# Performance work log

Hardware: AMD Instinct MI355X
Metric: run time of the kernel (lower is better)

The kernel has to match this reference:

```python
import jax, jax.numpy as jnp
import numpy as np

N_NODES = 100000
N_EDGES = 1600000
IN_C, HID, OUT_C = 16, 64, 1


def setup_inputs() -> dict:
    key = jax.random.key(0)
    ks = jax.random.split(key, 12)
    x = jax.random.normal(ks[0], (N_NODES, IN_C), dtype=jnp.float32)
    edge_index = jax.random.randint(ks[1], (2, N_EDGES), 0, N_NODES, dtype=jnp.int32)

    def lin(k, fan_in, fan_out):
        s = 1.0 / np.sqrt(fan_in)
        kw, kb = jax.random.split(k)
        W = jax.random.uniform(kw, (fan_in, fan_out), jnp.float32, -s, s)
        b = jax.random.uniform(kb, (fan_out,), jnp.float32, -s, s)
        return W, b

    W0, b0 = lin(ks[2], IN_C, HID)      # node_mlps[0]
    W1, b1 = lin(ks[3], HID, HID)       # node_mlps[1]
    W2, b2 = lin(ks[4], HID, OUT_C)     # node_mlps[2]
    M0, bM0 = lin(ks[5], 2 * HID, HID)  # message_mlps[0] (only one used for num_layers=3)
    return {"x": x, "edge_index": edge_index, "W0": W0, "b0": b0,
            "W1": W1, "b1": b1, "W2": W2, "b2": b2, "M0": M0, "bM0": bM0}


def _message_passing(h, src, dst, M, bM):
    # gather -> concat -> linear -> scatter-add -> degree normalize
    msgs = jnp.concatenate([h[src], h[dst]], axis=1) @ M + bM  # [E, HID]
    agg = jax.ops.segment_sum(msgs, dst, num_segments=N_NODES)  # [N, HID]
    deg = jax.ops.segment_sum(jnp.ones((src.shape[0],), h.dtype), dst,
                              num_segments=N_NODES)
    deg = jnp.clip(deg, 1.0, None)[:, None]
    return agg / deg


def reference(x, edge_index, W0, b0, W1, b1, W2, b2, M0, bM0):
    src, dst = edge_index[0], edge_index[1]
    h = jax.nn.relu(x @ W0 + b0)                  # node_mlps[0] (dropout = eval identity)
    h = h + _message_passing(h, src, dst, M0, bM0)
    h = jax.nn.relu(h @ W1 + b1)                  # node_mlps[1]
    return h @ W2 + b2                            # node_mlps[2], [N, 1]
```

## Files before the change

### kernel.cpp

```cpp
#include <hip/hip_runtime.h>

#define HID 64
#define IN_C 16

typedef __attribute__((ext_vector_type(8))) short short8;
typedef __attribute__((ext_vector_type(4))) float f32x4;

__device__ __forceinline__ float bitsf(unsigned u) { return __uint_as_float(u); }
__device__ __forceinline__ unsigned rne16(float f) {
    unsigned u = __float_as_uint(f);
    return (u + 0x7fffu + ((u >> 16) & 1u)) >> 16;
}
__device__ __forceinline__ float lanebcf(float v, int l) {
    return __int_as_float(__builtin_amdgcn_readlane(__float_as_int(v), l));
}
__device__ __forceinline__ float f4c(const float4& a, int c) {
    switch (c & 3) { case 0: return a.x; case 1: return a.y; case 2: return a.z; default: return a.w; }
}

__global__ void k_init(const float* __restrict__ M0, const float* __restrict__ W1,
                       const float* __restrict__ bM0, const float* __restrict__ b1,
                       ushort* __restrict__ WPhi, ushort* __restrict__ WPlo,
                       float* __restrict__ bias192) {
    int tid = blockIdx.x * 256 + threadIdx.x;
    if (tid >= 64 * 192) return;
    int cc = tid % 192;
    int k  = tid / 192;
    float w;
    if (cc < 64) {
        float a = 0.f;
#pragma unroll
        for (int m = 0; m < HID; ++m) a = fmaf(M0[k * HID + m], W1[m * HID + cc], a);
        w = a;
    } else if (cc < 128) {
        int c = cc - 64;
        float a = W1[k * HID + c];
#pragma unroll
        for (int m = 0; m < HID; ++m) a = fmaf(M0[(HID + k) * HID + m], W1[m * HID + c], a);
        w = a;
    } else {
        w = W1[k * HID + (cc - 128)];
    }
    unsigned wb = __float_as_uint(w);
    ushort hi = (ushort)(wb >> 16);
    float hif = __uint_as_float(wb & 0xffff0000u);
    ushort lo = (ushort)(__float_as_uint(w - hif) >> 16);
    int ct = cc >> 4, s = k >> 5, l = ((k >> 3) & 3) * 16 + (cc & 15), j = k & 7;
    int fi = ((ct * 2 + s) * 64 + l) * 8 + j;
    WPhi[fi] = hi;
    WPlo[fi] = lo;
    if (k == 0) {
        float bv;
        if (cc < 64) bv = 0.f;
        else if (cc < 128) {
            int c = cc - 64;
            float a = b1[c];
#pragma unroll
            for (int m = 0; m < HID; ++m) a = fmaf(bM0[m], W1[m * HID + c], a);
            bv = a;
        } else bv = b1[cc - 128];
        bias192[cc] = bv;
    }
}

__global__ __launch_bounds__(256) void k_pre_hist(
    const float* __restrict__ x, const float* __restrict__ W0, const float* __restrict__ b0,
    const ushort* __restrict__ WPhi, const ushort* __restrict__ WPlo,
    const float* __restrict__ bias192,
    ushort* __restrict__ zb, float* __restrict__ PQ, float* __restrict__ Pp, int N,
    const int* __restrict__ ei, int* __restrict__ bhT, int E, int B1, int NB1)
{
    __shared__ ushort hhi[64 * 64];
    __shared__ ushort hlo[64 * 64];

    if ((int)blockIdx.x < NB1) {
        int* h = reinterpret_cast<int*>(hhi);
        for (int i = threadIdx.x; i < B1; i += 256) h[i] = 0;
        __syncthreads();
        int CH = (E + NB1 - 1) / NB1;
        int e0 = blockIdx.x * CH;
        int e1 = min(e0 + CH, E);
        for (int e = e0 + (int)threadIdx.x; e < e1; e += 256)
            atomicAdd(&h[ei[E + e] >> 8], 1);
        __syncthreads();
        for (int i = threadIdx.x; i < B1; i += 256)
            bhT[(size_t)i * NB1 + blockIdx.x] = h[i];
        return;
    }

    int tid  = threadIdx.x;
    int lane = tid & 63;
    int w    = tid >> 6;
    int n0   = (blockIdx.x - NB1) * 64;

    float w0c[IN_C];
#pragma unroll
    for (int k = 0; k < IN_C; ++k) w0c[k] = W0[k * HID + lane];
    float b0l = b0[lane];

    short8 Whi[3][2], Wlo[3][2];
    float4 bias4[3];
#pragma unroll
    for (int i = 0; i < 3; ++i) {
        int ct = w * 3 + i;
#pragma unroll
        for (int s = 0; s < 2; ++s) {
            int fi = ((ct * 2 + s) * 64 + lane) * 8;
            Whi[i][s] = *reinterpret_cast<const short8*>(WPhi + fi);
            Wlo[i][s] = *reinterpret_cast<const short8*>(WPlo + fi);
        }
        bias4[i] = *reinterpret_cast<const float4*>(bias192 + ct * 16 + (lane >> 4) * 4);
    }

    int nx = n0 + w * 16 + (lane >> 2);
    float4 xq = make_float4(0.f, 0.f, 0.f, 0.f);
    if (nx < N) xq = *reinterpret_cast<const float4*>(x + (size_t)nx * IN_C + (lane & 3) * 4);

#pragma unroll
    for (int nn = 0; nn < 16; ++nn) {
        float acc = b0l;
#pragma unroll
        for (int k = 0; k < IN_C; ++k)
            acc = fmaf(lanebcf(f4c(xq, k & 3), 4 * nn + (k >> 2)), w0c[k], acc);
        float h = fmaxf(acc, 0.f);
        unsigned hb = __float_as_uint(h);
        ushort hi = (ushort)(hb >> 16);
        float hif = __uint_as_float(hb & 0xffff0000u);
        ushort lo = (ushort)(__float_as_uint(h - hif) >> 16);
        int nl = w * 16 + nn;
        int u  = ((lane >> 3) ^ (nl & 7));
        int off = nl * 64 + u * 8 + (lane & 7);
        hhi[off] = hi;
        hlo[off] = lo;
    }
    __syncthreads();

#pragma unroll
    for (int st = 0; st < 4; ++st) {
        int nloc = st * 16 + (lane & 15);
        short8 Ahi[2], Alo[2];
#pragma unroll
        for (int s = 0; s < 2; ++s) {
            int u = (s * 4 + (lane >> 4)) ^ (nloc & 7);
            int off = nloc * 64 + u * 8;
            Ahi[s] = *reinterpret_cast<const short8*>(hhi + off);
            Alo[s] = *reinterpret_cast<const short8*>(hlo + off);
        }
        int n = n0 + st * 16 + (lane & 15);
#pragma unroll
        for (int i = 0; i < 3; ++i) {
            int ct = w * 3 + i;
            f32x4 acc = {bias4[i].x, bias4[i].y, bias4[i].z, bias4[i].w};
#pragma unroll
            for (int s = 0; s < 2; ++s) {
                acc = __builtin_amdgcn_mfma_f32_16x16x32_bf16(Whi[i][s], Ahi[s], acc, 0, 0, 0);
                acc = __builtin_amdgcn_mfma_f32_16x16x32_bf16(Whi[i][s], Alo[s], acc, 0, 0, 0);
                acc = __builtin_amdgcn_mfma_f32_16x16x32_bf16(Wlo[i][s], Ahi[s], acc, 0, 0, 0);
                acc = __builtin_amdgcn_mfma_f32_16x16x32_bf16(Wlo[i][s], Alo[s], acc, 0, 0, 0);
            }
            if (n < N) {
                int chb = ct * 16 + (lane >> 4) * 4;
                if (chb < 64) {
                    uint2 pk;
                    pk.x = rne16(acc[0]) | (rne16(acc[1]) << 16);
                    pk.y = rne16(acc[2]) | (rne16(acc[3]) << 16);
                    *reinterpret_cast<uint2*>(zb + (size_t)n * HID + chb) = pk;
                } else if (chb < 128) {
                    float4 v = make_float4(acc[0], acc[1], acc[2], acc[3]);
                    *reinterpret_cast<float4*>(PQ + (size_t)n * HID + (chb - 64)) = v;
                } else {
                    float4 v = make_float4(acc[0], acc[1], acc[2], acc[3]);
                    *reinterpret_cast<float4*>(Pp + (size_t)n * HID + (chb - 128)) = v;
                }
            }
        }
    }
}

__global__ void k_scan1(const int* __restrict__ cnt, int* __restrict__ rs,
                        int* __restrict__ bsum, int M) {
    __shared__ int lds[256];
    int t = threadIdx.x;
    int base = blockIdx.x * 4096 + t * 16;
    int v[16];
    if (base + 16 <= M) {
#pragma unroll
        for (int u = 0; u < 4; ++u) {
            int4 w = *reinterpret_cast<const int4*>(cnt + base + u * 4);
            v[u * 4 + 0] = w.x; v[u * 4 + 1] = w.y; v[u * 4 + 2] = w.z; v[u * 4 + 3] = w.w;
        }
    } else {
#pragma unroll
        for (int u = 0; u < 16; ++u) v[u] = (base + u < M) ? cnt[base + u] : 0;
    }
    int run = 0;
#pragma unroll
    for (int u = 0; u < 16; ++u) { int tv = v[u]; v[u] = run; run += tv; }
    lds[t] = run;
    __syncthreads();
#pragma unroll
    for (int off = 1; off < 256; off <<= 1) {
        int xw = (t >= off) ? lds[t - off] : 0;
        __syncthreads();
        lds[t] += xw;
        __syncthreads();
    }
    int excl = lds[t] - run;
    if (t == 255) bsum[blockIdx.x] = lds[255];
#pragma unroll
    for (int u = 0; u < 16; ++u)
        if (base + u < M) rs[base + u] = excl + v[u];
}

__global__ void k_scan_add(int* __restrict__ rs, const int* __restrict__ bsum,
                           int NB, int M, int E) {
    __shared__ int lds[256];
    __shared__ int excl[256];
    int t = threadIdx.x;
    int v = (t < NB) ? bsum[t] : 0;
    lds[t] = v;
    __syncthreads();
#pragma unroll
    for (int off = 1; off < 256; off <<= 1) {
        int xw = (t >= off) ? lds[t - off] : 0;
        __syncthreads();
        lds[t] += xw;
        __syncthreads();
    }
    excl[t] = lds[t] - v;
    __syncthreads();
    int i = blockIdx.x * 256 + t;
    if (i < M) rs[i] += excl[i >> 12];
    if (i == 0) rs[M] = E;
}

__global__ __launch_bounds__(256) void k_p1scat(const int* __restrict__ ei, const int* __restrict__ off,
                                                unsigned* __restrict__ tmp, int E, int B1) {
    __shared__ int cur[1024];
    int NB1 = gridDim.x;
    for (int i = threadIdx.x; i < B1; i += 256)
        cur[i] = off[(size_t)i * NB1 + blockIdx.x];
    __syncthreads();
    int CH = (E + NB1 - 1) / NB1;
    int e0 = blockIdx.x * CH;
    int e1 = min(e0 + CH, E);
    for (int e = e0 + (int)threadIdx.x; e < e1; e += 256) {
        int s = ei[e];
        int d = ei[E + e];
        int pos = atomicAdd(&cur[d >> 8], 1);
        tmp[pos] = (unsigned)s | ((unsigned)(d & 255) << 24);
    }
}

__global__ __launch_bounds__(256) void k_p2(const unsigned* __restrict__ tmp, const int* __restrict__ off,
                                            int* __restrict__ rs, int* __restrict__ csr,
                                            int E, int N, int B1, int NB1) {
    __shared__ int h2[256];
    __shared__ int sc[256];
    __shared__ int cur[256];
    int b = blockIdx.x;
    int t = threadIdx.x;
    int bb0 = off[(size_t)b * NB1];
    int bb1 = off[(size_t)(b + 1) * NB1];

    h2[t] = 0;
    __syncthreads();
    for (int i = bb0 + t; i < bb1; i += 256)
        atomicAdd(&h2[tmp[i] >> 24], 1);
    __syncthreads();

    int v = h2[t];
    sc[t] = v;
    __syncthreads();
#pragma unroll
    for (int o = 1; o < 256; o <<= 1) {
        int xw = (t >= o) ? sc[t - o] : 0;
        __syncthreads();
        sc[t] += xw;
        __syncthreads();
    }
    int excl = sc[t] - v;

    int node = b * 256 + t;
    if (node < N) rs[node] = bb0 + excl;
    if (b == B1 - 1 && t == 0) rs[N] = E;
    cur[t] = bb0 + excl;
    __syncthreads();

    for (int i = bb0 + t; i < bb1; i += 256) {
        unsigned ed = tmp[i];
        int pos = atomicAdd(&cur[ed >> 24], 1);
        csr[pos] = (int)(ed & 0x00FFFFFFu);
    }
}

__global__ __launch_bounds__(256) void k_final(
    const ushort* __restrict__ zb, const float* __restrict__ PQ, const float* __restrict__ Pp,
    const int* __restrict__ rs, const int* __restrict__ csr,
    const float* __restrict__ W2, const float* __restrict__ b2,
    float* __restrict__ out, int N)
{
    int lane = threadIdx.x & 63;
    int g    = lane >> 4;
    int ql   = lane & 15;
    int oct  = ql & 7;
    int half = ql >> 3;
    int wid  = (blockIdx.x * 256 + threadIdx.x) >> 6;
    int nw   = (gridDim.x * 256) >> 6;

    int c0 = oct * 8 + half * 4;
    float4 w2v = *reinterpret_cast<const float4*>(W2 + c0);
    float b2s = b2[0];

    for (int n0 = wid * 4; n0 < N; n0 += nw * 4) {
        int ng   = n0 + g;
        bool okg = ng < N;

        int rv = okg ? rs[ng + half] : 0;
        int beg = __shfl(rv, g * 16 + 0);
        int end = __shfl(rv, g * 16 + 8);
        int deg = end - beg;
        int md = deg;
        md = max(md, __shfl_xor(md, 16));
        md = max(md, __shfl_xor(md, 32));

        float acc[8];
#pragma unroll
        for (int i = 0; i < 8; ++i) acc[i] = 0.f;

        for (int c = 0; c < md; c += 32) {
            int j0 = c + ql, j1 = c + 16 + ql;
            int ia = (j0 < deg) ? csr[beg + j0] : -1;
            int ib = (j1 < deg) ? csr[beg + j1] : -1;
#pragma unroll
            for (int tb = 0; tb < 4; ++tb) {
                if (tb > 0 && md <= c + 8 * tb) break;
                int srcs[4];
#pragma unroll
                for (int t4 = 0; t4 < 4; ++t4) {
                    int t = tb * 4 + t4;
                    int e = 2 * t + half;
                    srcs[t4] = __shfl(tb < 2 ? ia : ib, g * 16 + (e & 15));
                }
                uint4 rw[4];
#pragma unroll
                for (int t4 = 0; t4 < 4; ++t4) {
                    int s = srcs[t4] < 0 ? 0 : srcs[t4];
                    rw[t4] = *reinterpret_cast<const uint4*>(zb + (size_t)s * HID + oct * 8);
                }
#pragma unroll
                for (int t4 = 0; t4 < 4; ++t4) {
                    if (srcs[t4] >= 0) {
                        uint4 wv = rw[t4];
                        acc[0] += bitsf(wv.x << 16); acc[1] += bitsf(wv.x & 0xffff0000u);
                        acc[2] += bitsf(wv.y << 16); acc[3] += bitsf(wv.y & 0xffff0000u);
                        acc[4] += bitsf(wv.z << 16); acc[5] += bitsf(wv.z & 0xffff0000u);
                        acc[6] += bitsf(wv.w << 16); acc[7] += bitsf(wv.w & 0xffff0000u);
                    }
                }
            }
        }
#pragma unroll
        for (int i = 0; i < 8; ++i) acc[i] += __shfl_xor(acc[i], 8);

        float s0 = half ? acc[4] : acc[0];
        float s1 = half ? acc[5] : acc[1];
        float s2 = half ? acc[6] : acc[2];
        float s3 = half ? acc[7] : acc[3];

        float4 base = make_float4(0.f, 0.f, 0.f, 0.f);
        if (okg) {
            base = *reinterpret_cast<const float4*>(PQ + (size_t)ng * HID + c0);
            if (deg == 0)
                base = *reinterpret_cast<const float4*>(Pp + (size_t)ng * HID + c0);
        }
        float rcpd = (deg > 0) ? (1.f / (float)deg) : 0.f;
        float y0 = base.x + s0 * rcpd;
        float y1 = base.y + s1 * rcpd;
        float y2 = base.z + s2 * rcpd;
        float y3 = base.w + s3 * rcpd;

        float part = fmaxf(y0, 0.f) * w2v.x + fmaxf(y1, 0.f) * w2v.y +
                     fmaxf(y2, 0.f) * w2v.z + fmaxf(y3, 0.f) * w2v.w;
#pragma unroll
        for (int off = 1; off < 16; off <<= 1) part += __shfl_xor(part, off);
        if (ql == 0 && okg) out[ng] = part + b2s;
    }
}

extern "C" void kernel_launch(void* const* d_in, const int* in_sizes, int n_in,
                              void* d_out, int out_size, void* d_ws, size_t ws_size,
                              hipStream_t stream) {
    const float* x   = (const float*)d_in[0];
    const int*   ei  = (const int*)d_in[1];
    const float* W0  = (const float*)d_in[2];
    const float* b0  = (const float*)d_in[3];
    const float* W1  = (const float*)d_in[4];
    const float* b1  = (const float*)d_in[5];
    const float* W2  = (const float*)d_in[6];
    const float* b2  = (const float*)d_in[7];
    const float* M0  = (const float*)d_in[8];
    const float* bM0 = (const float*)d_in[9];

    int N = in_sizes[0] / IN_C;
    int E = in_sizes[1] / 2;
    int B1 = (N + 255) >> 8;
    int NB1 = 256;
    int M2 = B1 * NB1;
    int NB = (M2 + 4095) / 4096;

    ushort*   zb     = (ushort*)d_ws;
    float*    PQ     = (float*)(zb + (size_t)N * HID);
    float*    Pp     = PQ + (size_t)N * HID;
    ushort*   WPhi   = (ushort*)(Pp + (size_t)N * HID);
    ushort*   WPlo   = WPhi + 12288;
    float*    bias192= (float*)(WPlo + 12288);
    int*      bhT    = (int*)(bias192 + 192);
    int*      off    = bhT + (size_t)M2;
    int*      bsum   = off + (size_t)M2 + 1;
    int*      rs     = bsum + 256;
    unsigned* tmp    = (unsigned*)(rs + N + 1);
    int*      csr    = (int*)(tmp + (size_t)E);
    float*    out    = (float*)d_out;

    int npre = (N + 63) / 64;

    k_init<<<48, 256, 0, stream>>>(M0, W1, bM0, b1, WPhi, WPlo, bias192);
    k_pre_hist<<<NB1 + npre, 256, 0, stream>>>(x, W0, b0, WPhi, WPlo, bias192,
                                               zb, PQ, Pp, N, ei, bhT, E, B1, NB1);
    k_scan1<<<NB, 256, 0, stream>>>(bhT, off, bsum, M2);
    k_scan_add<<<(M2 + 255) / 256, 256, 0, stream>>>(off, bsum, NB, M2, E);
    k_p1scat<<<NB1, 256, 0, stream>>>(ei, off, tmp, E, B1);
    k_p2<<<B1, 256, 0, stream>>>(tmp, off, rs, csr, E, N, B1, NB1);
    k_final<<<2048, 256, 0, stream>>>(zb, PQ, Pp, rs, csr, W2, b2, out, N);
}
```

Baseline: 101.7 us.

## Fold block-sum scan into scatter kernels and store Pp as bf16

Removes the separate k_scan_add launch. k_p1scat and k_p2 now each rescan the small block-sum array in shared memory and add the block offset on the fly. The Pp buffer, which is read only for zero-degree nodes, is written and read as bf16 instead of fp32, halving its write traffic in the pre-pass. This saves one kernel launch plus a read-modify-write pass over the offset array, at the cost of redundant per-block scans and some precision loss on the Pp values.

```diff
diff --git a/kernel.cpp b/kernel.cpp
--- a/kernel.cpp
+++ b/kernel.cpp
@@ -67,7 +67,7 @@
     const float* __restrict__ x, const float* __restrict__ W0, const float* __restrict__ b0,
     const ushort* __restrict__ WPhi, const ushort* __restrict__ WPlo,
     const float* __restrict__ bias192,
-    ushort* __restrict__ zb, float* __restrict__ PQ, float* __restrict__ Pp, int N,
+    ushort* __restrict__ zb, float* __restrict__ PQ, ushort* __restrict__ Ppb, int N,
     const int* __restrict__ ei, int* __restrict__ bhT, int E, int B1, int NB1)
 {
     __shared__ ushort hhi[64 * 64];
@@ -169,8 +169,10 @@
                     float4 v = make_float4(acc[0], acc[1], acc[2], acc[3]);
                     *reinterpret_cast<float4*>(PQ + (size_t)n * HID + (chb - 64)) = v;
                 } else {
-                    float4 v = make_float4(acc[0], acc[1], acc[2], acc[3]);
-                    *reinterpret_cast<float4*>(Pp + (size_t)n * HID + (chb - 128)) = v;
+                    uint2 pk;
+                    pk.x = rne16(acc[0]) | (rne16(acc[1]) << 16);
+                    pk.y = rne16(acc[2]) | (rne16(acc[3]) << 16);
+                    *reinterpret_cast<uint2*>(Ppb + (size_t)n * HID + (chb - 128)) = pk;
                 }
             }
         }
@@ -212,39 +214,35 @@
         if (base + u < M) rs[base + u] = excl + v[u];
 }
 
-__global__ void k_scan_add(int* __restrict__ rs, const int* __restrict__ bsum,
-                           int NB, int M, int E) {
+__global__ __launch_bounds__(256) void k_p1scat(const int* __restrict__ ei, const int* __restrict__ off,
+                                                const int* __restrict__ bsum, int NBs,
+                                                unsigned* __restrict__ tmp, int E, int B1) {
+    __shared__ int cur[1024];
     __shared__ int lds[256];
     __shared__ int excl[256];
+    int NB1 = gridDim.x;
     int t = threadIdx.x;
-    int v = (t < NB) ? bsum[t] : 0;
+    int v = (t < NBs) ? bsum[t] : 0;
     lds[t] = v;
     __syncthreads();
 #pragma unroll
-    for (int off = 1; off < 256; off <<= 1) {
-        int xw = (t >= off) ? lds[t - off] : 0;
+    for (int o = 1; o < 256; o <<= 1) {
+        int xw = (t >= o) ? lds[t - o] : 0;
         __syncthreads();
         lds[t] += xw;
         __syncthreads();
     }
     excl[t] = lds[t] - v;
     __syncthreads();
-    int i = blockIdx.x * 256 + t;
-    if (i < M) rs[i] += excl[i >> 12];
-    if (i == 0) rs[M] = E;
-}
-
-__global__ __launch_bounds__(256) void k_p1scat(const int* __restrict__ ei, const int* __restrict__ off,
-                                                unsigned* __restrict__ tmp, int E, int B1) {
-    __shared__ int cur[1024];
-    int NB1 = gridDim.x;
-    for (int i = threadIdx.x; i < B1; i += 256)
-        cur[i] = off[(size_t)i * NB1 + blockIdx.x];
+    for (int i = t; i < B1; i += 256) {
+        int idx = i * NB1 + blockIdx.x;
+        cur[i] = off[idx] + excl[idx >> 12];
+    }
     __syncthreads();
     int CH = (E + NB1 - 1) / NB1;
     int e0 = blockIdx.x * CH;
     int e1 = min(e0 + CH, E);
-    for (int e = e0 + (int)threadIdx.x; e < e1; e += 256) {
+    for (int e = e0 + t; e < e1; e += 256) {
         int s = ei[e];
         int d = ei[E + e];
         int pos = atomicAdd(&cur[d >> 8], 1);
@@ -253,15 +251,40 @@
 }
 
 __global__ __launch_bounds__(256) void k_p2(const unsigned* __restrict__ tmp, const int* __restrict__ off,
+                                            const int* __restrict__ bsum, int NBs,
                                             int* __restrict__ rs, int* __restrict__ csr,
                                             int E, int N, int B1, int NB1) {
     __shared__ int h2[256];
     __shared__ int sc[256];
     __shared__ int cur[256];
+    __shared__ int bb[2];
     int b = blockIdx.x;
     int t = threadIdx.x;
-    int bb0 = off[(size_t)b * NB1];
-    int bb1 = off[(size_t)(b + 1) * NB1];
+
+    {
+        int v = (t < NBs) ? bsum[t] : 0;
+        sc[t] = v;
+        __syncthreads();
+#pragma unroll
+        for (int o = 1; o < 256; o <<= 1) {
+            int xw = (t >= o) ? sc[t - o] : 0;
+            __syncthreads();
+            sc[t] += xw;
+            __syncthreads();
+        }
+        if (t == 0) {
+            int i0 = b * NB1;
+            bb[0] = off[i0] + (sc[i0 >> 12] - ((i0 >> 12) < NBs ? bsum[i0 >> 12] : 0));
+        } else if (t == 1 && b < B1 - 1) {
+            int i1 = (b + 1) * NB1;
+            bb[1] = off[i1] + (sc[i1 >> 12] - ((i1 >> 12) < NBs ? bsum[i1 >> 12] : 0));
+        } else if (t == 1) {
+            bb[1] = E;
+        }
+    }
+    __syncthreads();
+    int bb0 = bb[0];
+    int bb1 = bb[1];
 
     h2[t] = 0;
     __syncthreads();
@@ -295,7 +318,7 @@
 }
 
 __global__ __launch_bounds__(256) void k_final(
-    const ushort* __restrict__ zb, const float* __restrict__ PQ, const float* __restrict__ Pp,
+    const ushort* __restrict__ zb, const float* __restrict__ PQ, const ushort* __restrict__ Ppb,
     const int* __restrict__ rs, const int* __restrict__ csr,
     const float* __restrict__ W2, const float* __restrict__ b2,
     float* __restrict__ out, int N)
@@ -371,8 +394,11 @@
         float4 base = make_float4(0.f, 0.f, 0.f, 0.f);
         if (okg) {
             base = *reinterpret_cast<const float4*>(PQ + (size_t)ng * HID + c0);
-            if (deg == 0)
-                base = *reinterpret_cast<const float4*>(Pp + (size_t)ng * HID + c0);
+            if (deg == 0) {
+                uint2 pb = *reinterpret_cast<const uint2*>(Ppb + (size_t)ng * HID + c0);
+                base.x = bitsf(pb.x << 16); base.y = bitsf(pb.x & 0xffff0000u);
+                base.z = bitsf(pb.y << 16); base.w = bitsf(pb.y & 0xffff0000u);
+            }
         }
         float rcpd = (deg > 0) ? (1.f / (float)deg) : 0.f;
         float y0 = base.x + s0 * rcpd;
@@ -407,17 +433,17 @@
     int B1 = (N + 255) >> 8;
     int NB1 = 256;
     int M2 = B1 * NB1;
-    int NB = (M2 + 4095) / 4096;
+    int NBs = (M2 + 4095) / 4096;
 
     ushort*   zb     = (ushort*)d_ws;
     float*    PQ     = (float*)(zb + (size_t)N * HID);
-    float*    Pp     = PQ + (size_t)N * HID;
-    ushort*   WPhi   = (ushort*)(Pp + (size_t)N * HID);
+    ushort*   Ppb    = (ushort*)(PQ + (size_t)N * HID);
+    ushort*   WPhi   = Ppb + (size_t)N * HID;
     ushort*   WPlo   = WPhi + 12288;
     float*    bias192= (float*)(WPlo + 12288);
     int*      bhT    = (int*)(bias192 + 192);
     int*      off    = bhT + (size_t)M2;
-    int*      bsum   = off + (size_t)M2 + 1;
+    int*      bsum   = off + (size_t)M2;
     int*      rs     = bsum + 256;
     unsigned* tmp    = (unsigned*)(rs + N + 1);
     int*      csr    = (int*)(tmp + (size_t)E);
@@ -427,10 +453,9 @@
 
     k_init<<<48, 256, 0, stream>>>(M0, W1, bM0, b1, WPhi, WPlo, bias192);
     k_pre_hist<<<NB1 + npre, 256, 0, stream>>>(x, W0, b0, WPhi, WPlo, bias192,
-                                               zb, PQ, Pp, N, ei, bhT, E, B1, NB1);
-    k_scan1<<<NB, 256, 0, stream>>>(bhT, off, bsum, M2);
-    k_scan_add<<<(M2 + 255) / 256, 256, 0, stream>>>(off, bsum, NB, M2, E);
-    k_p1scat<<<NB1, 256, 0, stream>>>(ei, off, tmp, E, B1);
-    k_p2<<<B1, 256, 0, stream>>>(tmp, off, rs, csr, E, N, B1, NB1);
-    k_final<<<2048, 256, 0, stream>>>(zb, PQ, Pp, rs, csr, W2, b2, out, N);
-}
+                                               zb, PQ, Ppb, N, ei, bhT, E, B1, NB1);
+    k_scan1<<<NBs, 256, 0, stream>>>(bhT, off, bsum, M2);
+    k_p1scat<<<NB1, 256, 0, stream>>>(ei, off, bsum, NBs, tmp, E, B1);
+    k_p2<<<B1, 256, 0, stream>>>(tmp, off, bsum, NBs, rs, csr, E, N, B1, NB1);
+    k_final<<<2048, 256, 0, stream>>>(zb, PQ, Ppb, rs, csr, W2, b2, out, N);
+}
```

New measurement: 101.8 us. About the same (+0.2%).
